# Performance work log

Measured on AMD Instinct MI355X. Metric: run time of the kernel, lower is better.

Reference implementation:

```python
import jax, jax.numpy as jnp
import numpy as np

NEG_BIG = 1e9  # additive mask magnitude from the original code


def setup_inputs() -> dict:
    key = jax.random.key(0)
    k1, k2, k3 = jax.random.split(key, 3)
    B, H, W, Cqk, Cv = 4, 64, 64, 256, 256
    return {
        "query": jax.random.normal(k1, (B, H, W, Cqk), dtype=jnp.float32),
        "key": jax.random.normal(k2, (B, H, W, Cqk), dtype=jnp.float32),
        "value": jax.random.normal(k3, (B, H, W, Cv), dtype=jnp.float32),
    }


def reference(query, key, value):
    B = query.shape[0]
    Cqk = key.shape[-1]
    Cv = value.shape[-1]
    out_spatial = query.shape[1:-1]

    q = query.reshape(B, -1, Cqk)   # [B, Sq, C]
    k = key.reshape(B, -1, Cqk)     # [B, S, C]
    v = value.reshape(B, -1, Cv)    # [B, S, Cv]
    Sq = q.shape[1]

    # PixelSNAIL causal mask: position i may attend to strictly earlier
    # positions j < i (row 0 attends to nothing -> zero output row).
    allowed = jnp.tril(jnp.ones((Sq, Sq), dtype=q.dtype), k=-1)  # [Sq, S]

    scale = 1.0 / jnp.sqrt(jnp.asarray(Cqk, dtype=q.dtype))
    scores = jnp.einsum("bqc,bkc->bqk", q, k) * scale  # [B, Sq, S]
    scores = scores - NEG_BIG * (1.0 - allowed)
    probs = jax.nn.softmax(scores, axis=-1) * allowed   # zero out masked probs
    mixed = jnp.einsum("bqk,bkv->bqv", probs, v)        # [B, Sq, Cv]
    return mixed.reshape((B,) + out_spatial + (Cv,))
```

## Files before the change

kernel.cpp:

```cpp
#include <hip/hip_runtime.h>

#define S_LEN 4096
#define DIM   256
#define QBLK  128
#define KVBLK 64
#define TILE_SH (KVBLK * DIM)
#define PER_B  1056
#define NBLK   256
#define TOT    4224

typedef __attribute__((ext_vector_type(4))) float f32x4;
typedef __attribute__((ext_vector_type(8))) short bf16x8;
typedef __attribute__((ext_vector_type(4))) unsigned short u16x4;
typedef __attribute__((ext_vector_type(8))) unsigned short u16x8;

__device__ __forceinline__ unsigned short f2bf(float x) {
    union { float f; unsigned u; } v; v.f = x;
    unsigned r = v.u + 0x7FFFu + ((v.u >> 16) & 1u);
    return (unsigned short)(r >> 16);
}
__device__ __forceinline__ float bf2f(unsigned short h) {
    union { unsigned u; float f; } v; v.u = ((unsigned)h) << 16;
    return v.f;
}

__device__ __forceinline__ void g2l16(const unsigned short* g, unsigned short* s) {
    __builtin_amdgcn_global_load_lds(
        (const __attribute__((address_space(1))) unsigned int*)g,
        (__attribute__((address_space(3))) unsigned int*)s, 16, 0, 0);
}

__device__ __forceinline__ int xcd_remap(int pos) {
    return ((pos & 7) >> 1) * 64 + (((pos >> 3) << 1) | (pos & 1));
}

__device__ __forceinline__ void decode_item(int x, int& b, int& qt, int& t) {
    b = x / PER_B;
    int r = x - b * PER_B;
    int q = (int)((__fsqrt_rn(4.0f * (float)r + 1.0f) - 1.0f) * 0.5f);
    while ((q + 1) * (q + 2) <= r) ++q;
    while (q * (q + 1) > r) --q;
    qt = q;
    t = r - q * (q + 1);
}

__global__ __launch_bounds__(256) void prepass(
        const float* __restrict__ K, const float* __restrict__ V,
        unsigned short* __restrict__ KW, unsigned short* __restrict__ VW) {
    __shared__ unsigned short vt[TILE_SH];
    const int tile = xcd_remap(blockIdx.x);
    const int tid  = threadIdx.x;
    const float* ks = K + (size_t)tile * (KVBLK * DIM);
    const float* vs = V + (size_t)tile * (KVBLK * DIM);

    char* kw = (char*)(KW + (size_t)tile * TILE_SH);
#pragma unroll
    for (int j = 0; j < 8; ++j) {
        int u = j * 256 + tid;
        int row = u >> 5, c8 = u & 31;
        f32x4 a  = *(const f32x4*)(ks + row * DIM + c8 * 8);
        f32x4 bb = *(const f32x4*)(ks + row * DIM + c8 * 8 + 4);
        u16x8 h;
        h[0] = f2bf(a[0]);  h[1] = f2bf(a[1]);  h[2] = f2bf(a[2]);  h[3] = f2bf(a[3]);
        h[4] = f2bf(bb[0]); h[5] = f2bf(bb[1]); h[6] = f2bf(bb[2]); h[7] = f2bf(bb[3]);
        unsigned off = (unsigned)(row * 512 + c8 * 16) ^ (unsigned)((row & 7) << 4);
        *(u16x8*)(kw + off) = h;
    }
    {
        int col = tid;
#pragma unroll
        for (int r8 = 0; r8 < 8; ++r8) {
            u16x8 h;
#pragma unroll
            for (int e = 0; e < 8; ++e) h[e] = f2bf(vs[(r8 * 8 + e) * DIM + col]);
            unsigned off = (unsigned)(col * 128 + r8 * 16) ^ (unsigned)((col & 7) << 4);
            *(u16x8*)((char*)vt + off) = h;
        }
    }
    __syncthreads();
    char* vw = (char*)(VW + (size_t)tile * TILE_SH);
#pragma unroll
    for (int j = 0; j < 8; ++j) {
        int u = j * 256 + tid;
        *(u16x8*)(vw + u * 16) = *(const u16x8*)((const char*)vt + u * 16);
    }
}

template<bool PACKED>
__global__ __launch_bounds__(512, 1) void attn_flash(
        const float* __restrict__ Qg, const unsigned short* __restrict__ KW,
        const unsigned short* __restrict__ VW, unsigned short* __restrict__ OP,
        float* __restrict__ ML, float* __restrict__ Og) {
    __shared__ unsigned short Ksh[2][TILE_SH];
    __shared__ unsigned short VshT[2][TILE_SH];
    __shared__ unsigned short Psh[8][16 * KVBLK];
    __shared__ float lsh[8][16];

    const int tid = threadIdx.x;
    const int w   = tid >> 6;
    const int l   = tid & 63;
    const int l15 = l & 15;
    const int lg  = l >> 4;
    const int p   = w >> 1;
    const int h   = w & 1;
    const int qga = 2 * p, qgb = 2 * p + 1;

    int s, e, ilog = blockIdx.x;
    if (PACKED) {
        ilog = xcd_remap(blockIdx.x);
        s = (33 * ilog) >> 1;
        e = (33 * (ilog + 1)) >> 1;
    } else {
        const int b0 = blockIdx.x & 3, q0 = blockIdx.x >> 2;
        s = b0 * PER_B + q0 * (q0 + 1);
        e = s + 2 * q0 + 2;
    }

    int b, qt, t;
    decode_item(s, b, qt, t);
    int tstart = t;
    bool firstSec = true;

    bf16x8 qf[8];
    {
        const float* qp = Qg + (size_t)(b * S_LEN + qt * QBLK + w * 16 + l15) * DIM + lg * 8;
#pragma unroll
        for (int ks = 0; ks < 8; ++ks) {
            f32x4 a = *(const f32x4*)(qp + ks * 32);
            f32x4 c = *(const f32x4*)(qp + ks * 32 + 4);
            bf16x8 f;
            f[0] = (short)f2bf(a[0] * 0.0625f); f[1] = (short)f2bf(a[1] * 0.0625f);
            f[2] = (short)f2bf(a[2] * 0.0625f); f[3] = (short)f2bf(a[3] * 0.0625f);
            f[4] = (short)f2bf(c[0] * 0.0625f); f[5] = (short)f2bf(c[1] * 0.0625f);
            f[6] = (short)f2bf(c[2] * 0.0625f); f[7] = (short)f2bf(c[3] * 0.0625f);
            qf[ks] = f;
        }
    }

    f32x4 acc[2][8];
#pragma unroll
    for (int qi = 0; qi < 2; ++qi)
#pragma unroll
        for (int i2 = 0; i2 < 8; ++i2) acc[qi][i2] = (f32x4)0.0f;
    float lrun = 0.f;

    {
        const unsigned short* kimg = KW + (size_t)(b * 64 + t) * TILE_SH + w * 2048 + l * 8;
        const unsigned short* vimg = VW + (size_t)(b * 64 + t) * TILE_SH + w * 2048 + l * 8;
        unsigned short* kd = &Ksh[0][w * 2048];
        unsigned short* vd = &VshT[0][w * 2048];
#pragma unroll
        for (int i = 0; i < 4; ++i) {
            g2l16(kimg + i * 512, kd + i * 512);
            g2l16(vimg + i * 512, vd + i * 512);
        }
    }
    __syncthreads();

    int x = s, cur = 0;
    while (true) {
        const bool have_next = (x + 1 < e);
        int nb = b, nqt = qt, ntt = t + 1;
        const bool secEnd = !have_next || (ntt >= 2 * qt + 2);
        if (have_next) {
            if (ntt >= 2 * qt + 2) decode_item(x + 1, nb, nqt, ntt);
            const unsigned short* kimg = KW + (size_t)(nb * 64 + ntt) * TILE_SH + w * 2048 + l * 8;
            const unsigned short* vimg = VW + (size_t)(nb * 64 + ntt) * TILE_SH + w * 2048 + l * 8;
            unsigned short* kd = &Ksh[cur ^ 1][w * 2048];
            unsigned short* vd = &VshT[cur ^ 1][w * 2048];
#pragma unroll
            for (int i = 0; i < 4; ++i) {
                g2l16(kimg + i * 512, kd + i * 512);
                g2l16(vimg + i * 512, vd + i * 512);
            }
        }

        const int qbase  = qt * QBLK;
        const bool skipq  = (t * KVBLK >= qbase + w * 16 + 16);
        const bool skippv = (t * KVBLK >= qbase + qgb * 16 + 16);
        const bool mskq   = (t * KVBLK + KVBLK - 1 >= qbase + w * 16);

        u16x4 pk[4];
        if (!skipq) {
            f32x4 sacc[4];
#pragma unroll
            for (int j = 0; j < 4; ++j) sacc[j] = (f32x4)0.0f;
            __builtin_amdgcn_s_setprio(1);
#pragma unroll
            for (int ks = 0; ks < 8; ++ks) {
#pragma unroll
                for (int jt = 0; jt < 4; ++jt) {
                    int j = jt * 16 + l15;
                    unsigned off = (unsigned)(j * 512 + (ks * 32 + lg * 8) * 2);
                    off ^= (unsigned)((j & 7) << 4);
                    bf16x8 kb = *(const bf16x8*)((const char*)Ksh[cur] + off);
                    sacc[jt] = __builtin_amdgcn_mfma_f32_16x16x32_bf16(kb, qf[ks], sacc[jt], 0, 0, 0);
                }
            }
            __builtin_amdgcn_s_setprio(0);
            if (mskq) {
                const int qg = qbase + w * 16 + l15;
#pragma unroll
                for (int jt = 0; jt < 4; ++jt)
#pragma unroll
                    for (int rr = 0; rr < 4; ++rr) {
                        int kg = t * KVBLK + jt * 16 + lg * 4 + rr;
                        if (kg >= qg) sacc[jt][rr] = -3e38f;
                    }
            }
            float ls = 0.f;
#pragma unroll
            for (int jt = 0; jt < 4; ++jt) {
                f32x4 pv;
#pragma unroll
                for (int rr = 0; rr < 4; ++rr) {
                    float pe = __expf(sacc[jt][rr]);
                    pv[rr] = pe;
                    ls += pe;
                }
                pk[jt].x = f2bf(pv[0]); pk[jt].y = f2bf(pv[1]);
                pk[jt].z = f2bf(pv[2]); pk[jt].w = f2bf(pv[3]);
            }
            ls += __shfl_xor(ls, 16);
            ls += __shfl_xor(ls, 32);
            lrun += ls;
        } else {
#pragma unroll
            for (int jt = 0; jt < 4; ++jt) { pk[jt].x = 0; pk[jt].y = 0; pk[jt].z = 0; pk[jt].w = 0; }
        }
        {
            char* pw = (char*)&Psh[w][0];
            unsigned base = (unsigned)(l15 * 128 + lg * 8) ^ (unsigned)((l15 & 7) << 4);
#pragma unroll
            for (int jt = 0; jt < 4; ++jt)
                *(u16x4*)(pw + (base ^ (unsigned)(jt * 32))) = pk[jt];
        }
        __syncthreads();

        if (!skippv) {
            __builtin_amdgcn_s_setprio(1);
#pragma unroll
            for (int ks = 0; ks < 2; ++ks) {
                unsigned poff = (unsigned)(l15 * 128 + ks * 64 + lg * 16);
                poff ^= (unsigned)((l15 & 7) << 4);
                bf16x8 pa_ = *(const bf16x8*)((const char*)&Psh[qga][0] + poff);
                bf16x8 pb_ = *(const bf16x8*)((const char*)&Psh[qgb][0] + poff);
#pragma unroll
                for (int ni = 0; ni < 8; ++ni) {
                    int nt = h * 8 + ni;
                    unsigned voff = (unsigned)((nt * 16 + l15) * 128 + ks * 64 + lg * 16);
                    voff ^= (unsigned)((l15 & 7) << 4);
                    bf16x8 va = *(const bf16x8*)((const char*)VshT[cur] + voff);
                    acc[0][ni] = __builtin_amdgcn_mfma_f32_16x16x32_bf16(va, pa_, acc[0][ni], 0, 0, 0);
                    acc[1][ni] = __builtin_amdgcn_mfma_f32_16x16x32_bf16(va, pb_, acc[1][ni], 0, 0, 0);
                }
            }
            __builtin_amdgcn_s_setprio(0);
        }
        __syncthreads();

        if (secEnd) {
            if (lg == 0) lsh[w][l15] = lrun;
            __syncthreads();
            const bool complete = (tstart == 0) && (t == 2 * qt + 1);
            if (complete) {
                float la = lsh[qga][l15], lb = lsh[qgb][l15];
                float rla = (la > 0.f) ? (1.0f / la) : 0.f;
                float rlb = (lb > 0.f) ? (1.0f / lb) : 0.f;
                float* oa = Og + (size_t)(b * S_LEN + qbase + qga * 16 + l15) * DIM;
                float* ob = Og + (size_t)(b * S_LEN + qbase + qgb * 16 + l15) * DIM;
#pragma unroll
                for (int ni = 0; ni < 8; ++ni) {
                    int nt = h * 8 + ni;
                    f32x4 o0 = acc[0][ni] * rla;
                    f32x4 o1 = acc[1][ni] * rlb;
                    *(f32x4*)(oa + nt * 16 + lg * 4) = o0;
                    *(f32x4*)(ob + nt * 16 + lg * 4) = o1;
                }
            } else {
                const int slot = 2 * ilog + (firstSec ? 0 : 1);
                unsigned short* opa = OP + (size_t)slot * (QBLK * DIM)
                                         + (size_t)(qga * 16 + l15) * DIM;
                unsigned short* opb = OP + (size_t)slot * (QBLK * DIM)
                                         + (size_t)(qgb * 16 + l15) * DIM;
#pragma unroll
                for (int ni = 0; ni < 8; ++ni) {
                    int nt = h * 8 + ni;
                    u16x4 pa2, pb2;
                    pa2.x = f2bf(acc[0][ni][0]); pa2.y = f2bf(acc[0][ni][1]);
                    pa2.z = f2bf(acc[0][ni][2]); pa2.w = f2bf(acc[0][ni][3]);
                    pb2.x = f2bf(acc[1][ni][0]); pb2.y = f2bf(acc[1][ni][1]);
                    pb2.z = f2bf(acc[1][ni][2]); pb2.w = f2bf(acc[1][ni][3]);
                    *(u16x4*)(opa + nt * 16 + lg * 4) = pa2;
                    *(u16x4*)(opb + nt * 16 + lg * 4) = pb2;
                }
                if (lg == 0) {
                    float* mlp = ML + (size_t)slot * (2 * QBLK);
                    mlp[(w * 16 + l15) * 2]     = 0.0f;
                    mlp[(w * 16 + l15) * 2 + 1] = lrun;
                }
            }
            if (!have_next) break;
            {
                const float* qp = Qg + (size_t)(nb * S_LEN + nqt * QBLK + w * 16 + l15) * DIM + lg * 8;
#pragma unroll
                for (int ks = 0; ks < 8; ++ks) {
                    f32x4 a = *(const f32x4*)(qp + ks * 32);
                    f32x4 c = *(const f32x4*)(qp + ks * 32 + 4);
                    bf16x8 f;
                    f[0] = (short)f2bf(a[0] * 0.0625f); f[1] = (short)f2bf(a[1] * 0.0625f);
                    f[2] = (short)f2bf(a[2] * 0.0625f); f[3] = (short)f2bf(a[3] * 0.0625f);
                    f[4] = (short)f2bf(c[0] * 0.0625f); f[5] = (short)f2bf(c[1] * 0.0625f);
                    f[6] = (short)f2bf(c[2] * 0.0625f); f[7] = (short)f2bf(c[3] * 0.0625f);
                    qf[ks] = f;
                }
            }
#pragma unroll
            for (int qi = 0; qi < 2; ++qi)
#pragma unroll
                for (int i2 = 0; i2 < 8; ++i2) acc[qi][i2] = (f32x4)0.0f;
            lrun = 0.f;
            firstSec = false; tstart = 0;
        }
        ++x; b = nb; qt = nqt; t = ntt; cur ^= 1;
    }
}

__global__ __launch_bounds__(256) void attn_combine(
        const unsigned short* __restrict__ OP, const float* __restrict__ ML,
        float* __restrict__ Og) {
    const int id = blockIdx.x;
    const int rg = id & 3;
    const int bq = id >> 2;
    const int b  = bq >> 5;
    const int qt = bq & 31;
    const int A  = b * PER_B + qt * (qt + 1);
    const int E  = A + 2 * qt + 2;
    const int j0 = (2 * A + 1) / 33;
    const int j1 = (2 * E - 1) / 33;
    if (j0 >= j1) return;
    const int C = j1 - j0 + 1;

    int slots[6];
    for (int c = 0; c < C; ++c) {
        int j  = j0 + c;
        int sj = (33 * j) >> 1;
        slots[c] = 2 * j + ((sj >= A) ? 0 : 1);
    }

    const int tid = threadIdx.x;
    float* outb = Og + ((size_t)(b * S_LEN + qt * QBLK)) * DIM;
#pragma unroll
    for (int jj = 0; jj < 4; ++jj) {
        int u   = jj * 256 + tid;
        int row = rg * 32 + (u >> 5);
        int d8  = u & 31;
        float M = -1e30f;
        for (int c = 0; c < C; ++c)
            M = fmaxf(M, ML[(size_t)slots[c] * (2 * QBLK) + row * 2]);
        float L = 0.f;
        float o[8];
#pragma unroll
        for (int e2 = 0; e2 < 8; ++e2) o[e2] = 0.f;
        for (int c = 0; c < C; ++c) {
            float mm = ML[(size_t)slots[c] * (2 * QBLK) + row * 2];
            float ll = ML[(size_t)slots[c] * (2 * QBLK) + row * 2 + 1];
            float sc = __expf(mm - M);
            L += ll * sc;
            u16x8 ph = *(const u16x8*)(OP + ((size_t)slots[c] * QBLK + row) * DIM + d8 * 8);
#pragma unroll
            for (int e2 = 0; e2 < 8; ++e2) o[e2] += sc * bf2f(ph[e2]);
        }
        float rl = (L > 0.f) ? (1.0f / L) : 0.f;
        f32x4 o0, o1;
        o0[0] = o[0] * rl; o0[1] = o[1] * rl; o0[2] = o[2] * rl; o0[3] = o[3] * rl;
        o1[0] = o[4] * rl; o1[1] = o[5] * rl; o1[2] = o[6] * rl; o1[3] = o[7] * rl;
        *(f32x4*)(outb + (size_t)row * DIM + d8 * 8)     = o0;
        *(f32x4*)(outb + (size_t)row * DIM + d8 * 8 + 4) = o1;
    }
}

extern "C" void kernel_launch(void* const* d_in, const int* in_sizes, int n_in,
                              void* d_out, int out_size, void* d_ws, size_t ws_size,
                              hipStream_t stream) {
    const float* q = (const float*)d_in[0];
    const float* k = (const float*)d_in[1];
    const float* v = (const float*)d_in[2];
    float* o = (float*)d_out;

    const size_t imgShorts = (size_t)256 * TILE_SH;
    const size_t IMG = 2 * imgShorts * sizeof(unsigned short);
    unsigned short* KW = (unsigned short*)d_ws;
    unsigned short* VW = KW + imgShorts;

    const int nslots = 2 * NBLK;
    const size_t need = IMG
        + (size_t)nslots * (QBLK * DIM) * 2
        + (size_t)nslots * (2 * QBLK) * 4;
    if (ws_size < IMG) return;

    hipLaunchKernelGGL(prepass, dim3(256), dim3(256), 0, stream, k, v, KW, VW);
    if (ws_size >= need) {
        unsigned short* OP = (unsigned short*)((char*)d_ws + IMG);
        float* ML = (float*)(OP + (size_t)nslots * (QBLK * DIM));
        hipLaunchKernelGGL((attn_flash<true>), dim3(NBLK), dim3(512), 0, stream,
                           q, KW, VW, OP, ML, o);
        hipLaunchKernelGGL(attn_combine, dim3(512), dim3(256), 0, stream,
                           OP, ML, o);
    } else {
        hipLaunchKernelGGL((attn_flash<false>), dim3(128), dim3(512), 0, stream,
                           q, KW, VW, (unsigned short*)nullptr, (float*)nullptr, o);
    }
}
```

Before: 98.37 us.

## Software-pipeline PV matmul one tile behind QK and split K/V prefetch

```diff
diff --git a/kernel.cpp b/kernel.cpp
--- a/kernel.cpp
+++ b/kernel.cpp
@@ -42,6 +42,20 @@
     while (q * (q + 1) > r) --q;
     qt = q;
     t = r - q * (q + 1);
+}
+
+__device__ __forceinline__ void load_q(const float* qp, bf16x8* qf) {
+#pragma unroll
+    for (int ks = 0; ks < 8; ++ks) {
+        f32x4 a = *(const f32x4*)(qp + ks * 32);
+        f32x4 c = *(const f32x4*)(qp + ks * 32 + 4);
+        bf16x8 f;
+        f[0] = (short)f2bf(a[0] * 0.0625f); f[1] = (short)f2bf(a[1] * 0.0625f);
+        f[2] = (short)f2bf(a[2] * 0.0625f); f[3] = (short)f2bf(a[3] * 0.0625f);
+        f[4] = (short)f2bf(c[0] * 0.0625f); f[5] = (short)f2bf(c[1] * 0.0625f);
+        f[6] = (short)f2bf(c[2] * 0.0625f); f[7] = (short)f2bf(c[3] * 0.0625f);
+        qf[ks] = f;
+    }
 }
 
 __global__ __launch_bounds__(256) void prepass(
@@ -122,20 +136,7 @@
     bool firstSec = true;
 
     bf16x8 qf[8];
-    {
-        const float* qp = Qg + (size_t)(b * S_LEN + qt * QBLK + w * 16 + l15) * DIM + lg * 8;
-#pragma unroll
-        for (int ks = 0; ks < 8; ++ks) {
-            f32x4 a = *(const f32x4*)(qp + ks * 32);
-            f32x4 c = *(const f32x4*)(qp + ks * 32 + 4);
-            bf16x8 f;
-            f[0] = (short)f2bf(a[0] * 0.0625f); f[1] = (short)f2bf(a[1] * 0.0625f);
-            f[2] = (short)f2bf(a[2] * 0.0625f); f[3] = (short)f2bf(a[3] * 0.0625f);
-            f[4] = (short)f2bf(c[0] * 0.0625f); f[5] = (short)f2bf(c[1] * 0.0625f);
-            f[6] = (short)f2bf(c[2] * 0.0625f); f[7] = (short)f2bf(c[3] * 0.0625f);
-            qf[ks] = f;
-        }
-    }
+    load_q(Qg + (size_t)(b * S_LEN + qt * QBLK + w * 16 + l15) * DIM + lg * 8, qf);
 
     f32x4 acc[2][8];
 #pragma unroll
@@ -143,12 +144,34 @@
 #pragma unroll
         for (int i2 = 0; i2 < 8; ++i2) acc[qi][i2] = (f32x4)0.0f;
     float lrun = 0.f;
+    bool pvalid = false, pskippv = true;
+
+    auto do_pv = [&](int par) {
+        __builtin_amdgcn_s_setprio(1);
+#pragma unroll
+        for (int ks = 0; ks < 2; ++ks) {
+            unsigned poff = (unsigned)(l15 * 128 + ks * 64 + lg * 16);
+            poff ^= (unsigned)((l15 & 7) << 4);
+            bf16x8 pa_ = *(const bf16x8*)((const char*)&Psh[qga][0] + poff);
+            bf16x8 pb_ = *(const bf16x8*)((const char*)&Psh[qgb][0] + poff);
+#pragma unroll
+            for (int ni = 0; ni < 8; ++ni) {
+                int nt = h * 8 + ni;
+                unsigned voff = (unsigned)((nt * 16 + l15) * 128 + ks * 64 + lg * 16);
+                voff ^= (unsigned)((l15 & 7) << 4);
+                bf16x8 va = *(const bf16x8*)((const char*)VshT[par] + voff);
+                acc[0][ni] = __builtin_amdgcn_mfma_f32_16x16x32_bf16(va, pa_, acc[0][ni], 0, 0, 0);
+                acc[1][ni] = __builtin_amdgcn_mfma_f32_16x16x32_bf16(va, pb_, acc[1][ni], 0, 0, 0);
+            }
+        }
+        __builtin_amdgcn_s_setprio(0);
+    };
 
     {
         const unsigned short* kimg = KW + (size_t)(b * 64 + t) * TILE_SH + w * 2048 + l * 8;
         const unsigned short* vimg = VW + (size_t)(b * 64 + t) * TILE_SH + w * 2048 + l * 8;
-        unsigned short* kd = &Ksh[0][w * 2048];
-        unsigned short* vd = &VshT[0][w * 2048];
+        unsigned short* kd = &Ksh[s & 1][w * 2048];
+        unsigned short* vd = &VshT[s & 1][w * 2048];
 #pragma unroll
         for (int i = 0; i < 4; ++i) {
             g2l16(kimg + i * 512, kd + i * 512);
@@ -157,34 +180,30 @@
     }
     __syncthreads();
 
-    int x = s, cur = 0;
+    int x = s;
     while (true) {
+        const int cur = x & 1;
         const bool have_next = (x + 1 < e);
         int nb = b, nqt = qt, ntt = t + 1;
         const bool secEnd = !have_next || (ntt >= 2 * qt + 2);
+        if (have_next && ntt >= 2 * qt + 2) decode_item(x + 1, nb, nqt, ntt);
+
         if (have_next) {
-            if (ntt >= 2 * qt + 2) decode_item(x + 1, nb, nqt, ntt);
             const unsigned short* kimg = KW + (size_t)(nb * 64 + ntt) * TILE_SH + w * 2048 + l * 8;
-            const unsigned short* vimg = VW + (size_t)(nb * 64 + ntt) * TILE_SH + w * 2048 + l * 8;
             unsigned short* kd = &Ksh[cur ^ 1][w * 2048];
-            unsigned short* vd = &VshT[cur ^ 1][w * 2048];
-#pragma unroll
-            for (int i = 0; i < 4; ++i) {
-                g2l16(kimg + i * 512, kd + i * 512);
-                g2l16(vimg + i * 512, vd + i * 512);
-            }
-        }
-
-        const int qbase  = qt * QBLK;
-        const bool skipq  = (t * KVBLK >= qbase + w * 16 + 16);
-        const bool skippv = (t * KVBLK >= qbase + qgb * 16 + 16);
-        const bool mskq   = (t * KVBLK + KVBLK - 1 >= qbase + w * 16);
-
-        u16x4 pk[4];
+#pragma unroll
+            for (int i = 0; i < 4; ++i) g2l16(kimg + i * 512, kd + i * 512);
+        }
+
+        const int qbase    = qt * QBLK;
+        const bool skipq    = (t * KVBLK >= qbase + w * 16 + 16);
+        const bool skippv_x = (t * KVBLK >= qbase + qgb * 16 + 16);
+        const bool mskq     = (t * KVBLK + KVBLK - 1 >= qbase + w * 16);
+
+        f32x4 sacc[4];
+#pragma unroll
+        for (int j = 0; j < 4; ++j) sacc[j] = (f32x4)0.0f;
         if (!skipq) {
-            f32x4 sacc[4];
-#pragma unroll
-            for (int j = 0; j < 4; ++j) sacc[j] = (f32x4)0.0f;
             __builtin_amdgcn_s_setprio(1);
 #pragma unroll
             for (int ks = 0; ks < 8; ++ks) {
@@ -198,6 +217,23 @@
                 }
             }
             __builtin_amdgcn_s_setprio(0);
+        }
+        if (pvalid && !pskippv) do_pv(cur ^ 1);
+
+        asm volatile("s_waitcnt lgkmcnt(0)" ::: "memory");
+        __builtin_amdgcn_sched_barrier(0);
+        __builtin_amdgcn_s_barrier();
+        __builtin_amdgcn_sched_barrier(0);
+
+        if (have_next) {
+            const unsigned short* vimg = VW + (size_t)(nb * 64 + ntt) * TILE_SH + w * 2048 + l * 8;
+            unsigned short* vd = &VshT[cur ^ 1][w * 2048];
+#pragma unroll
+            for (int i = 0; i < 4; ++i) g2l16(vimg + i * 512, vd + i * 512);
+        }
+
+        u16x4 pk[4];
+        if (!skipq) {
             if (mskq) {
                 const int qg = qbase + w * 16 + l15;
 #pragma unroll
@@ -235,31 +271,18 @@
             for (int jt = 0; jt < 4; ++jt)
                 *(u16x4*)(pw + (base ^ (unsigned)(jt * 32))) = pk[jt];
         }
-        __syncthreads();
-
-        if (!skippv) {
-            __builtin_amdgcn_s_setprio(1);
-#pragma unroll
-            for (int ks = 0; ks < 2; ++ks) {
-                unsigned poff = (unsigned)(l15 * 128 + ks * 64 + lg * 16);
-                poff ^= (unsigned)((l15 & 7) << 4);
-                bf16x8 pa_ = *(const bf16x8*)((const char*)&Psh[qga][0] + poff);
-                bf16x8 pb_ = *(const bf16x8*)((const char*)&Psh[qgb][0] + poff);
-#pragma unroll
-                for (int ni = 0; ni < 8; ++ni) {
-                    int nt = h * 8 + ni;
-                    unsigned voff = (unsigned)((nt * 16 + l15) * 128 + ks * 64 + lg * 16);
-                    voff ^= (unsigned)((l15 & 7) << 4);
-                    bf16x8 va = *(const bf16x8*)((const char*)VshT[cur] + voff);
-                    acc[0][ni] = __builtin_amdgcn_mfma_f32_16x16x32_bf16(va, pa_, acc[0][ni], 0, 0, 0);
-                    acc[1][ni] = __builtin_amdgcn_mfma_f32_16x16x32_bf16(va, pb_, acc[1][ni], 0, 0, 0);
-                }
-            }
-            __builtin_amdgcn_s_setprio(0);
-        }
-        __syncthreads();
 
         if (secEnd) {
+            asm volatile("s_waitcnt vmcnt(0) lgkmcnt(0)" ::: "memory");
+        } else {
+            asm volatile("s_waitcnt vmcnt(4) lgkmcnt(0)" ::: "memory");
+        }
+        __builtin_amdgcn_sched_barrier(0);
+        __builtin_amdgcn_s_barrier();
+        __builtin_amdgcn_sched_barrier(0);
+
+        if (secEnd) {
+            if (!skippv_x) do_pv(cur);
             if (lg == 0) lsh[w][l15] = lrun;
             __syncthreads();
             const bool complete = (tstart == 0) && (t == 2 * qt + 1);
@@ -301,28 +324,18 @@
                 }
             }
             if (!have_next) break;
-            {
-                const float* qp = Qg + (size_t)(nb * S_LEN + nqt * QBLK + w * 16 + l15) * DIM + lg * 8;
-#pragma unroll
-                for (int ks = 0; ks < 8; ++ks) {
-                    f32x4 a = *(const f32x4*)(qp + ks * 32);
-                    f32x4 c = *(const f32x4*)(qp + ks * 32 + 4);
-                    bf16x8 f;
-                    f[0] = (short)f2bf(a[0] * 0.0625f); f[1] = (short)f2bf(a[1] * 0.0625f);
-                    f[2] = (short)f2bf(a[2] * 0.0625f); f[3] = (short)f2bf(a[3] * 0.0625f);
-                    f[4] = (short)f2bf(c[0] * 0.0625f); f[5] = (short)f2bf(c[1] * 0.0625f);
-                    f[6] = (short)f2bf(c[2] * 0.0625f); f[7] = (short)f2bf(c[3] * 0.0625f);
-                    qf[ks] = f;
-                }
-            }
+            load_q(Qg + (size_t)(nb * S_LEN + nqt * QBLK + w * 16 + l15) * DIM + lg * 8, qf);
 #pragma unroll
             for (int qi = 0; qi < 2; ++qi)
 #pragma unroll
                 for (int i2 = 0; i2 < 8; ++i2) acc[qi][i2] = (f32x4)0.0f;
             lrun = 0.f;
+            pvalid = false; pskippv = true;
             firstSec = false; tstart = 0;
-        }
-        ++x; b = nb; qt = nqt; t = ntt; cur ^= 1;
+        } else {
+            pvalid = true; pskippv = skippv_x;
+        }
+        ++x; b = nb; qt = nqt; t = ntt;
     }
 }
 
```

Result: no change. 100.0 us (+1.7%).
